# Kernel tuning notes

Measured on AMD Instinct MI355X. Metric: run time of the kernel, lower is better.

Reference implementation:

```python
import jax, jax.numpy as jnp
import numpy as np

N = 60000          # users
M = 40000          # items
NODES = N + M
D = 64             # embedding_dim
NLAYERS = 3        # layers = [64, 64, 64]
NNZ = 3_200_000    # nnz of L_I (avg degree 32)
B = 1024           # batch_size
NEG_SLOPE = 0.2


def setup_inputs() -> dict:
    key = jax.random.key(0)
    ks = jax.random.split(key, 12)
    edge_row = jax.random.randint(ks[0], (NNZ,), 0, NODES, dtype=jnp.int32)
    edge_col = jax.random.randint(ks[1], (NNZ,), 0, NODES, dtype=jnp.int32)
    # Laplacian values are small positive normalized weights
    edge_val = jax.random.uniform(ks[2], (NNZ,), dtype=jnp.float32) * (1.0 / 32.0)
    embed_user = jax.random.normal(ks[3], (N, D), dtype=jnp.float32) * 0.1
    embed_item = jax.random.normal(ks[4], (M, D), dtype=jnp.float32) * 0.1
    W1 = jax.random.normal(ks[5], (NLAYERS, D, D), dtype=jnp.float32) * 0.1
    W2 = jax.random.normal(ks[6], (NLAYERS, D, D), dtype=jnp.float32) * 0.1
    b1 = jax.random.normal(ks[7], (NLAYERS, 1, D), dtype=jnp.float32) * 0.1
    b2 = jax.random.normal(ks[8], (NLAYERS, 1, D), dtype=jnp.float32) * 0.1
    sampled_users = jax.random.randint(ks[9], (B,), 0, N, dtype=jnp.int32)
    observed_items_idx = jax.random.randint(ks[10], (B,), 0, M, dtype=jnp.int32)
    unobserved_items_idx = jax.random.randint(ks[11], (B,), 0, M, dtype=jnp.int32)
    return {
        "edge_row": edge_row, "edge_col": edge_col, "edge_val": edge_val,
        "embed_user": embed_user, "embed_item": embed_item,
        "W1": W1, "W2": W2, "b1": b1, "b2": b2,
        "sampled_users": sampled_users,
        "observed_items_idx": observed_items_idx,
        "unobserved_items_idx": unobserved_items_idx,
    }


def _spmm(row, col, val, x):
    # sparse (NODES x NODES) @ dense (NODES x D) via gather + segment-sum
    return jax.ops.segment_sum(val[:, None] * x[col], row, num_segments=NODES)


def reference(edge_row, edge_col, edge_val, embed_user, embed_item,
              W1, W2, b1, b2,
              sampled_users, observed_items_idx, unobserved_items_idx):
    x = jnp.concatenate([embed_user, embed_item], axis=0)  # (NODES, D)
    reprs = [x]
    for i in range(NLAYERS):
        lie = _spmm(edge_row, edge_col, edge_val, x)        # L_I @ E
        left = lie @ W1[i] + b1[i]
        right = (x * lie) @ W2[i] + b2[i]
        x = jax.nn.leaky_relu(left + right, negative_slope=NEG_SLOPE)
        reprs.append(x)
    final_reprs = jnp.concatenate(reprs, axis=1)            # (NODES, D*(NLAYERS+1))
    users_, items_ = final_reprs[:N], final_reprs[N:]
    return (users_[sampled_users],
            items_[observed_items_idx],
            items_[unobserved_items_idx])
```

## Files before the change

### kernel.cpp

```cpp
#include <hip/hip_runtime.h>

#define NN    60000
#define NODES 100000
#define DD    64
#define NNZ   3200000
#define BB    1024
#define NEG   0.2f
#define RPB   196
#define NBUCK 511
#define EPB   8192
#define NPB   ((NNZ + EPB - 1) / EPB)
#define CAP   7000
#define BCAP  7168
#define NSEG  13
#define KEYN  (NSEG * RPB)
#define SPB   (KEYN + 1)

__global__ __launch_bounds__(256) void k_init_x(const float* __restrict__ eu,
                                                const float* __restrict__ ei,
                                                float* __restrict__ x,
                                                int* __restrict__ gcur) {
    int i = blockIdx.x * 256 + threadIdx.x;
    if (i < NBUCK) gcur[i] = i * CAP;
    const int TOT = NODES * DD / 4;
    if (i >= TOT) return;
    const int UE = NN * DD / 4;
    float4 v = (i < UE) ? ((const float4*)eu)[i] : ((const float4*)ei)[i - UE];
    ((float4*)x)[i] = v;
}

__global__ __launch_bounds__(512) void k_place(const int* __restrict__ row,
                                               const int* __restrict__ col,
                                               const float* __restrict__ val,
                                               int* __restrict__ gcur,
                                               int2* __restrict__ bulk) {
    __shared__ int rows_l[EPB];
    __shared__ unsigned short perm[EPB];
    __shared__ int h[NBUCK], bloc[NBUCK], bcur[NBUCK], gseg[NBUCK];
    __shared__ int sc[512];
    int t = threadIdx.x;
    if (t < NBUCK) h[t] = 0;
    __syncthreads();
    int base = blockIdx.x * EPB;
    int n = min(EPB, NNZ - base);
    for (int k = t; k < n; k += 512) {
        int r = row[base + k];
        rows_l[k] = r;
        atomicAdd(&h[r / RPB], 1);
    }
    __syncthreads();
    {
        int v = (t < NBUCK) ? h[t] : 0;
        sc[t] = v;
        __syncthreads();
        for (int off = 1; off < 512; off <<= 1) {
            int u = (t >= off) ? sc[t - off] : 0;
            __syncthreads();
            sc[t] += u;
            __syncthreads();
        }
        if (t < NBUCK) {
            int ex = sc[t] - v;
            bloc[t] = ex;
            bcur[t] = ex;
            gseg[t] = v ? atomicAdd(&gcur[t], v) : 0;
        }
    }
    __syncthreads();
    for (int k = t; k < n; k += 512) {
        int p = atomicAdd(&bcur[rows_l[k] / RPB], 1);
        perm[p] = (unsigned short)k;
    }
    __syncthreads();
    for (int j = t; j < n; j += 512) {
        int k = perm[j];
        int r = rows_l[k];
        int b = r / RPB;
        int addr = gseg[b] + (j - bloc[b]);
        bulk[addr] = make_int2(((r - b * RPB) << 17) | col[base + k],
                               __float_as_int(val[base + k]));
    }
}

__global__ __launch_bounds__(512) void k_csr(const int* __restrict__ gcur,
                                             int2* __restrict__ bulk,
                                             int* __restrict__ starts) {
    __shared__ int2 eds[BCAP];
    __shared__ int cnt[KEYN], pos[KEYN];
    __shared__ int part[512];
    int b = blockIdx.x, t = threadIdx.x;
    int lo = b * CAP;
    int n = gcur[b] - lo;
    for (int k = t; k < KEYN; k += 512) cnt[k] = 0;
    __syncthreads();
    for (int i = t; i < n; i += 512) {
        int2 ed = bulk[lo + i];
        eds[i] = ed;
        int lr = ed.x >> 17, c = ed.x & 0x1FFFF;
        atomicAdd(&cnt[(c >> 13) * RPB + lr], 1);
    }
    __syncthreads();
    int run = 0;
#pragma unroll
    for (int j = 0; j < 5; ++j) {
        int k = t * 5 + j;
        if (k < KEYN) { pos[k] = run; run += cnt[k]; }
    }
    part[t] = run;
    __syncthreads();
    for (int off = 1; off < 512; off <<= 1) {
        int u = (t >= off) ? part[t - off] : 0;
        __syncthreads();
        part[t] += u;
        __syncthreads();
    }
    int poff = part[t] - run;
#pragma unroll
    for (int j = 0; j < 5; ++j) {
        int k = t * 5 + j;
        if (k < KEYN) pos[k] += poff;
    }
    __syncthreads();
    for (int k = t; k < KEYN; k += 512) {
        starts[b * SPB + k] = lo + pos[k];
        cnt[k] = pos[k];
    }
    if (t == 0) starts[b * SPB + KEYN] = lo + n;
    __syncthreads();
    for (int i = t; i < n; i += 512) {
        int2 ed = eds[i];
        int lr = ed.x >> 17, c = ed.x & 0x1FFFF;
        int p = atomicAdd(&cnt[(c >> 13) * RPB + lr], 1);
        bulk[lo + p] = ed;
    }
}

template <int PIPE>
__global__ __launch_bounds__(1024) void k_cspmm(const int* __restrict__ starts,
                                                const int2* __restrict__ cv,
                                                const float* __restrict__ x,
                                                float* __restrict__ lie) {
    __shared__ float acc[RPB * DD];
    int t = threadIdx.x, b = blockIdx.x;
    float4* av = (float4*)acc;
    for (int i = t; i < RPB * 16; i += 1024) av[i] = make_float4(0.f, 0.f, 0.f, 0.f);
    __syncthreads();
    int lane = t & 63;
    int wid = __builtin_amdgcn_readfirstlane(t >> 6);
    int r0 = (wid * RPB) >> 4;
    int r1 = ((wid + 1) * RPB) >> 4;
    int sb = b * SPB;
    for (int seg = 0; seg < NSEG; ++seg) {
        int s = starts[sb + seg * RPB + r0];
        int e = starts[sb + seg * RPB + r1];
        int cur = -1;
        float f = 0.f;
        if constexpr (PIPE == 0) {
            int g = s;
            for (; g + 8 <= e; g += 8) {
                int2 ee[8];
#pragma unroll
                for (int j = 0; j < 8; ++j) ee[j] = cv[g + j];
                float xv[8];
#pragma unroll
                for (int j = 0; j < 8; ++j) xv[j] = x[(ee[j].x & 0x1FFFF) * DD + lane];
#pragma unroll
                for (int j = 0; j < 8; ++j) {
                    int r = ee[j].x >> 17;
                    if (r != cur) {
                        if (cur >= 0) acc[cur * DD + lane] += f;
                        cur = r; f = 0.f;
                    }
                    f = fmaf(__int_as_float(ee[j].y), xv[j], f);
                }
            }
            for (; g < e; ++g) {
                int2 ed = cv[g];
                float xg = x[(ed.x & 0x1FFFF) * DD + lane];
                int r = ed.x >> 17;
                if (r != cur) {
                    if (cur >= 0) acc[cur * DD + lane] += f;
                    cur = r; f = 0.f;
                }
                f = fmaf(__int_as_float(ed.y), xg, f);
            }
        } else {
            int2 emA[8], emB[8];
            float xwA[8], xwB[8];
#define LDM(S, gg) { _Pragma("unroll") \
    for (int j = 0; j < 8; ++j) em##S[j] = cv[(gg) + j]; }
#define GTH(S) { _Pragma("unroll") \
    for (int j = 0; j < 8; ++j) xw##S[j] = x[(em##S[j].x & 0x1FFFF) * DD + lane]; }
#define CNS(S) { _Pragma("unroll") \
    for (int j = 0; j < 8; ++j) { \
        int r = em##S[j].x >> 17; \
        if (r != cur) { if (cur >= 0) acc[cur * DD + lane] += f; cur = r; f = 0.f; } \
        f = fmaf(__int_as_float(em##S[j].y), xw##S[j], f); } }
            int nb = (e - s) >> 3;
            if (nb > 0) {
                LDM(A, s) GTH(A)
                int ld = 1;
                for (;;) {
                    if (ld < nb) { LDM(B, s + ld * 8) GTH(B) ++ld; CNS(A) }
                    else         { CNS(A) break; }
                    if (ld < nb) { LDM(A, s + ld * 8) GTH(A) ++ld; CNS(B) }
                    else         { CNS(B) break; }
                }
            }
#undef LDM
#undef GTH
#undef CNS
            for (int g = s + nb * 8; g < e; ++g) {
                int2 ed = cv[g];
                float xg = x[(ed.x & 0x1FFFF) * DD + lane];
                int r = ed.x >> 17;
                if (r != cur) {
                    if (cur >= 0) acc[cur * DD + lane] += f;
                    cur = r; f = 0.f;
                }
                f = fmaf(__int_as_float(ed.y), xg, f);
            }
        }
        if (cur >= 0) acc[cur * DD + lane] += f;
    }
    __syncthreads();
    int row0 = b * RPB;
    for (int i = t; i < RPB * 16; i += 1024) {
        int gr = row0 + (i >> 4);
        if (gr < NODES) ((float4*)lie)[gr * 16 + (i & 15)] = av[i];
    }
}

__global__ __launch_bounds__(256) void k_gemm(float* __restrict__ x,
                                              const float* __restrict__ lie,
                                              const float* __restrict__ W1,
                                              const float* __restrict__ W2,
                                              const float* __restrict__ b1,
                                              const float* __restrict__ b2) {
    __shared__ float A1[64 * 64];
    __shared__ float A2[64 * 64];
    __shared__ float Ws1[64 * 64];
    __shared__ float Ws2[64 * 64];

    const int t = threadIdx.x;
    const int row0 = blockIdx.x * 64;

    {
        const float4* w1v = (const float4*)W1;
        const float4* w2v = (const float4*)W2;
        float4* s1v = (float4*)Ws1;
        float4* s2v = (float4*)Ws2;
#pragma unroll
        for (int q = 0; q < 4; ++q) {
            s1v[q * 256 + t] = w1v[q * 256 + t];
            s2v[q * 256 + t] = w2v[q * 256 + t];
        }
    }
#pragma unroll
    for (int q = 0; q < 4; ++q) {
        int f4 = q * 256 + t;
        int rl = f4 >> 4;
        int c4 = f4 & 15;
        int gr = row0 + rl;
        float4 lv = make_float4(0.f, 0.f, 0.f, 0.f);
        float4 xv = make_float4(0.f, 0.f, 0.f, 0.f);
        if (gr < NODES) {
            lv = *(const float4*)&lie[gr * DD + c4 * 4];
            xv = *(const float4*)&x[gr * DD + c4 * 4];
        }
        int sg = c4 ^ (rl & 15);
        ((float4*)A1)[rl * 16 + sg] = lv;
        ((float4*)A2)[rl * 16 + sg] = make_float4(lv.x * xv.x, lv.y * xv.y,
                                                  lv.z * xv.z, lv.w * xv.w);
    }
    __syncthreads();

    const int tx = t & 15;
    const int ty = t >> 4;
    float bs[4];
    {
        float4 bb1 = *(const float4*)&b1[tx * 4];
        float4 bb2 = *(const float4*)&b2[tx * 4];
        bs[0] = bb1.x + bb2.x; bs[1] = bb1.y + bb2.y;
        bs[2] = bb1.z + bb2.z; bs[3] = bb1.w + bb2.w;
    }
    float acc[4][4];
#pragma unroll
    for (int i = 0; i < 4; ++i)
#pragma unroll
        for (int j = 0; j < 4; ++j) acc[i][j] = bs[j];

    for (int k4 = 0; k4 < 16; ++k4) {
        float4 a1[4], a2[4];
#pragma unroll
        for (int i = 0; i < 4; ++i) {
            int r = ty * 4 + i;
            int sg = k4 ^ (r & 15);
            a1[i] = ((const float4*)A1)[r * 16 + sg];
            a2[i] = ((const float4*)A2)[r * 16 + sg];
        }
#pragma unroll
        for (int kk = 0; kk < 4; ++kk) {
            float4 w1 = ((const float4*)Ws1)[(k4 * 4 + kk) * 16 + tx];
            float4 w2 = ((const float4*)Ws2)[(k4 * 4 + kk) * 16 + tx];
#pragma unroll
            for (int i = 0; i < 4; ++i) {
                float av1 = (&a1[i].x)[kk];
                float av2 = (&a2[i].x)[kk];
                acc[i][0] = fmaf(av1, w1.x, fmaf(av2, w2.x, acc[i][0]));
                acc[i][1] = fmaf(av1, w1.y, fmaf(av2, w2.y, acc[i][1]));
                acc[i][2] = fmaf(av1, w1.z, fmaf(av2, w2.z, acc[i][2]));
                acc[i][3] = fmaf(av1, w1.w, fmaf(av2, w2.w, acc[i][3]));
            }
        }
    }
#pragma unroll
    for (int i = 0; i < 4; ++i) {
        int gr = row0 + ty * 4 + i;
        if (gr < NODES) {
            float4 o;
            o.x = acc[i][0] >= 0.f ? acc[i][0] : NEG * acc[i][0];
            o.y = acc[i][1] >= 0.f ? acc[i][1] : NEG * acc[i][1];
            o.z = acc[i][2] >= 0.f ? acc[i][2] : NEG * acc[i][2];
            o.w = acc[i][3] >= 0.f ? acc[i][3] : NEG * acc[i][3];
            *(float4*)&x[gr * DD + tx * 4] = o;
        }
    }
}

__global__ __launch_bounds__(256) void k_gather(const float* __restrict__ x,
                                                const int* __restrict__ su,
                                                const int* __restrict__ oi,
                                                const int* __restrict__ ui,
                                                float* __restrict__ out, int layer) {
    int w    = (blockIdx.x * 256 + threadIdx.x) >> 6;
    int lane = threadIdx.x & 63;
    if (w >= 3 * BB) return;
    int g = w >> 10, b = w & 1023;
    int node = (g == 0) ? su[b] : (NN + ((g == 1) ? oi[b] : ui[b]));
    out[w * 256 + layer * 64 + lane] = x[node * DD + lane];
}

extern "C" void kernel_launch(void* const* d_in, const int* in_sizes, int n_in,
                              void* d_out, int out_size, void* d_ws, size_t ws_size,
                              hipStream_t stream) {
    const int*   edge_row = (const int*)d_in[0];
    const int*   edge_col = (const int*)d_in[1];
    const float* edge_val = (const float*)d_in[2];
    const float* eu = (const float*)d_in[3];
    const float* ei = (const float*)d_in[4];
    const float* W1 = (const float*)d_in[5];
    const float* W2 = (const float*)d_in[6];
    const float* b1 = (const float*)d_in[7];
    const float* b2 = (const float*)d_in[8];
    const int*   su = (const int*)d_in[9];
    const int*   oi = (const int*)d_in[10];
    const int*   ui = (const int*)d_in[11];
    float* out = (float*)d_out;

    float* x      = (float*)d_ws;
    float* lie    = x + NODES * DD;
    int2*  bulk   = (int2*)(lie + NODES * DD);
    int*   gcur   = (int*)(bulk + NBUCK * CAP);
    int*   starts = gcur + NBUCK + 1;

    k_init_x<<<(NODES * DD / 4 + 255) / 256, 256, 0, stream>>>(eu, ei, x, gcur);
    k_gather<<<(3 * BB * 64 + 255) / 256, 256, 0, stream>>>(x, su, oi, ui, out, 0);

    k_place<<<NPB, 512, 0, stream>>>(edge_row, edge_col, edge_val, gcur, bulk);
    k_csr<<<NBUCK, 512, 0, stream>>>(gcur, bulk, starts);

    for (int l = 0; l < 3; ++l) {
        if (l == 1)
            k_cspmm<1><<<NBUCK, 1024, 0, stream>>>(starts, bulk, x, lie);
        else
            k_cspmm<0><<<NBUCK, 1024, 0, stream>>>(starts, bulk, x, lie);
        k_gemm<<<(NODES + 63) / 64, 256, 0, stream>>>(x, lie,
                                                      W1 + l * 4096, W2 + l * 4096,
                                                      b1 + l * 64,  b2 + l * 64);
        k_gather<<<(3 * BB * 64 + 255) / 256, 256, 0, stream>>>(x, su, oi, ui, out, l + 1);
    }
}
```

Before: 520.8 us.

## Fuse SpMM with dense layer transform using ping-pong x buffers

Merges the sparse aggregation kernel and the dense W1/W2 GEMM into one kernel. Each block computes its rows of L·E in shared memory and then applies both weight matrices, bias and leaky ReLU directly. Double-buffered x arrays replace the in-place update. This removes the lie intermediate round-trip through global memory and one launch per layer, and uses the pipelined gather variant for all layers. In exchange the GEMM stage now reads weights from global/L1 per FMA without register tiling and has fewer blocks (511) than the old GEMM kernel.

Measured after the change: 1.617 ms. 210% more time.

```diff
diff --git a/kernel.cpp b/kernel.cpp
--- a/kernel.cpp
+++ b/kernel.cpp
@@ -135,11 +135,14 @@
     }
 }
 
-template <int PIPE>
-__global__ __launch_bounds__(1024) void k_cspmm(const int* __restrict__ starts,
+__global__ __launch_bounds__(1024) void k_fused(const int* __restrict__ starts,
                                                 const int2* __restrict__ cv,
-                                                const float* __restrict__ x,
-                                                float* __restrict__ lie) {
+                                                const float* __restrict__ xs,
+                                                float* __restrict__ xd,
+                                                const float* __restrict__ W1,
+                                                const float* __restrict__ W2,
+                                                const float* __restrict__ b1,
+                                                const float* __restrict__ b2) {
     __shared__ float acc[RPB * DD];
     int t = threadIdx.x, b = blockIdx.x;
     float4* av = (float4*)acc;
@@ -155,175 +158,86 @@
         int e = starts[sb + seg * RPB + r1];
         int cur = -1;
         float f = 0.f;
-        if constexpr (PIPE == 0) {
-            int g = s;
-            for (; g + 8 <= e; g += 8) {
-                int2 ee[8];
-#pragma unroll
-                for (int j = 0; j < 8; ++j) ee[j] = cv[g + j];
-                float xv[8];
-#pragma unroll
-                for (int j = 0; j < 8; ++j) xv[j] = x[(ee[j].x & 0x1FFFF) * DD + lane];
-#pragma unroll
-                for (int j = 0; j < 8; ++j) {
-                    int r = ee[j].x >> 17;
-                    if (r != cur) {
-                        if (cur >= 0) acc[cur * DD + lane] += f;
-                        cur = r; f = 0.f;
-                    }
-                    f = fmaf(__int_as_float(ee[j].y), xv[j], f);
-                }
-            }
-            for (; g < e; ++g) {
-                int2 ed = cv[g];
-                float xg = x[(ed.x & 0x1FFFF) * DD + lane];
-                int r = ed.x >> 17;
-                if (r != cur) {
-                    if (cur >= 0) acc[cur * DD + lane] += f;
-                    cur = r; f = 0.f;
-                }
-                f = fmaf(__int_as_float(ed.y), xg, f);
-            }
-        } else {
-            int2 emA[8], emB[8];
-            float xwA[8], xwB[8];
+        int2 emA[8], emB[8];
+        float xwA[8], xwB[8];
 #define LDM(S, gg) { _Pragma("unroll") \
     for (int j = 0; j < 8; ++j) em##S[j] = cv[(gg) + j]; }
 #define GTH(S) { _Pragma("unroll") \
-    for (int j = 0; j < 8; ++j) xw##S[j] = x[(em##S[j].x & 0x1FFFF) * DD + lane]; }
+    for (int j = 0; j < 8; ++j) xw##S[j] = xs[(em##S[j].x & 0x1FFFF) * DD + lane]; }
 #define CNS(S) { _Pragma("unroll") \
     for (int j = 0; j < 8; ++j) { \
         int r = em##S[j].x >> 17; \
         if (r != cur) { if (cur >= 0) acc[cur * DD + lane] += f; cur = r; f = 0.f; } \
         f = fmaf(__int_as_float(em##S[j].y), xw##S[j], f); } }
-            int nb = (e - s) >> 3;
-            if (nb > 0) {
-                LDM(A, s) GTH(A)
-                int ld = 1;
-                for (;;) {
-                    if (ld < nb) { LDM(B, s + ld * 8) GTH(B) ++ld; CNS(A) }
-                    else         { CNS(A) break; }
-                    if (ld < nb) { LDM(A, s + ld * 8) GTH(A) ++ld; CNS(B) }
-                    else         { CNS(B) break; }
-                }
-            }
+        int nb = (e - s) >> 3;
+        if (nb > 0) {
+            LDM(A, s) GTH(A)
+            int ld = 1;
+            for (;;) {
+                if (ld < nb) { LDM(B, s + ld * 8) GTH(B) ++ld; CNS(A) }
+                else         { CNS(A) break; }
+                if (ld < nb) { LDM(A, s + ld * 8) GTH(A) ++ld; CNS(B) }
+                else         { CNS(B) break; }
+            }
+        }
 #undef LDM
 #undef GTH
 #undef CNS
-            for (int g = s + nb * 8; g < e; ++g) {
-                int2 ed = cv[g];
-                float xg = x[(ed.x & 0x1FFFF) * DD + lane];
-                int r = ed.x >> 17;
-                if (r != cur) {
-                    if (cur >= 0) acc[cur * DD + lane] += f;
-                    cur = r; f = 0.f;
-                }
-                f = fmaf(__int_as_float(ed.y), xg, f);
-            }
+        for (int g = s + nb * 8; g < e; ++g) {
+            int2 ed = cv[g];
+            float xg = xs[(ed.x & 0x1FFFF) * DD + lane];
+            int r = ed.x >> 17;
+            if (r != cur) {
+                if (cur >= 0) acc[cur * DD + lane] += f;
+                cur = r; f = 0.f;
+            }
+            f = fmaf(__int_as_float(ed.y), xg, f);
         }
         if (cur >= 0) acc[cur * DD + lane] += f;
     }
     __syncthreads();
-    int row0 = b * RPB;
-    for (int i = t; i < RPB * 16; i += 1024) {
-        int gr = row0 + (i >> 4);
-        if (gr < NODES) ((float4*)lie)[gr * 16 + (i & 15)] = av[i];
-    }
-}
-
-__global__ __launch_bounds__(256) void k_gemm(float* __restrict__ x,
-                                              const float* __restrict__ lie,
-                                              const float* __restrict__ W1,
-                                              const float* __restrict__ W2,
-                                              const float* __restrict__ b1,
-                                              const float* __restrict__ b2) {
-    __shared__ float A1[64 * 64];
-    __shared__ float A2[64 * 64];
-    __shared__ float Ws1[64 * 64];
-    __shared__ float Ws2[64 * 64];
-
-    const int t = threadIdx.x;
-    const int row0 = blockIdx.x * 64;
 
     {
+        const int row0 = b * RPB;
+        const int tx = t & 15;
+        const int ty = t >> 4;
         const float4* w1v = (const float4*)W1;
         const float4* w2v = (const float4*)W2;
-        float4* s1v = (float4*)Ws1;
-        float4* s2v = (float4*)Ws2;
-#pragma unroll
-        for (int q = 0; q < 4; ++q) {
-            s1v[q * 256 + t] = w1v[q * 256 + t];
-            s2v[q * 256 + t] = w2v[q * 256 + t];
-        }
-    }
-#pragma unroll
-    for (int q = 0; q < 4; ++q) {
-        int f4 = q * 256 + t;
-        int rl = f4 >> 4;
-        int c4 = f4 & 15;
-        int gr = row0 + rl;
-        float4 lv = make_float4(0.f, 0.f, 0.f, 0.f);
-        float4 xv = make_float4(0.f, 0.f, 0.f, 0.f);
-        if (gr < NODES) {
-            lv = *(const float4*)&lie[gr * DD + c4 * 4];
-            xv = *(const float4*)&x[gr * DD + c4 * 4];
-        }
-        int sg = c4 ^ (rl & 15);
-        ((float4*)A1)[rl * 16 + sg] = lv;
-        ((float4*)A2)[rl * 16 + sg] = make_float4(lv.x * xv.x, lv.y * xv.y,
-                                                  lv.z * xv.z, lv.w * xv.w);
-    }
-    __syncthreads();
-
-    const int tx = t & 15;
-    const int ty = t >> 4;
-    float bs[4];
-    {
-        float4 bb1 = *(const float4*)&b1[tx * 4];
-        float4 bb2 = *(const float4*)&b2[tx * 4];
-        bs[0] = bb1.x + bb2.x; bs[1] = bb1.y + bb2.y;
-        bs[2] = bb1.z + bb2.z; bs[3] = bb1.w + bb2.w;
-    }
-    float acc[4][4];
-#pragma unroll
-    for (int i = 0; i < 4; ++i)
-#pragma unroll
-        for (int j = 0; j < 4; ++j) acc[i][j] = bs[j];
-
-    for (int k4 = 0; k4 < 16; ++k4) {
-        float4 a1[4], a2[4];
-#pragma unroll
-        for (int i = 0; i < 4; ++i) {
-            int r = ty * 4 + i;
-            int sg = k4 ^ (r & 15);
-            a1[i] = ((const float4*)A1)[r * 16 + sg];
-            a2[i] = ((const float4*)A2)[r * 16 + sg];
-        }
-#pragma unroll
-        for (int kk = 0; kk < 4; ++kk) {
-            float4 w1 = ((const float4*)Ws1)[(k4 * 4 + kk) * 16 + tx];
-            float4 w2 = ((const float4*)Ws2)[(k4 * 4 + kk) * 16 + tx];
-#pragma unroll
-            for (int i = 0; i < 4; ++i) {
-                float av1 = (&a1[i].x)[kk];
-                float av2 = (&a2[i].x)[kk];
-                acc[i][0] = fmaf(av1, w1.x, fmaf(av2, w2.x, acc[i][0]));
-                acc[i][1] = fmaf(av1, w1.y, fmaf(av2, w2.y, acc[i][1]));
-                acc[i][2] = fmaf(av1, w1.z, fmaf(av2, w2.z, acc[i][2]));
-                acc[i][3] = fmaf(av1, w1.w, fmaf(av2, w2.w, acc[i][3]));
-            }
-        }
-    }
-#pragma unroll
-    for (int i = 0; i < 4; ++i) {
-        int gr = row0 + ty * 4 + i;
-        if (gr < NODES) {
-            float4 o;
-            o.x = acc[i][0] >= 0.f ? acc[i][0] : NEG * acc[i][0];
-            o.y = acc[i][1] >= 0.f ? acc[i][1] : NEG * acc[i][1];
-            o.z = acc[i][2] >= 0.f ? acc[i][2] : NEG * acc[i][2];
-            o.w = acc[i][3] >= 0.f ? acc[i][3] : NEG * acc[i][3];
-            *(float4*)&x[gr * DD + tx * 4] = o;
+        float4 b1v = ((const float4*)b1)[tx];
+        float4 b2v = ((const float4*)b2)[tx];
+        float4 bb = make_float4(b1v.x + b2v.x, b1v.y + b2v.y,
+                                b1v.z + b2v.z, b1v.w + b2v.w);
+        int nr = (ty < RPB - 192) ? 4 : 3;
+        for (int i = 0; i < nr; ++i) {
+            int lr = ty + i * 64;
+            int gr = row0 + lr;
+            bool live = (gr < NODES);
+            float4 o = bb;
+            const float4* lrow = (const float4*)&acc[lr * DD];
+            const float4* xrow = (const float4*)&xs[(live ? gr : 0) * DD];
+#pragma unroll
+            for (int k4 = 0; k4 < 16; ++k4) {
+                float4 l4 = lrow[k4];
+                float4 x4 = xrow[k4];
+#pragma unroll
+                for (int kk = 0; kk < 4; ++kk) {
+                    float lk = (&l4.x)[kk];
+                    float ak = lk * (&x4.x)[kk];
+                    float4 w1r = w1v[(k4 * 4 + kk) * 16 + tx];
+                    float4 w2r = w2v[(k4 * 4 + kk) * 16 + tx];
+                    o.x = fmaf(lk, w1r.x, fmaf(ak, w2r.x, o.x));
+                    o.y = fmaf(lk, w1r.y, fmaf(ak, w2r.y, o.y));
+                    o.z = fmaf(lk, w1r.z, fmaf(ak, w2r.z, o.z));
+                    o.w = fmaf(lk, w1r.w, fmaf(ak, w2r.w, o.w));
+                }
+            }
+            if (live) {
+                o.x = o.x >= 0.f ? o.x : NEG * o.x;
+                o.y = o.y >= 0.f ? o.y : NEG * o.y;
+                o.z = o.z >= 0.f ? o.z : NEG * o.z;
+                o.w = o.w >= 0.f ? o.w : NEG * o.w;
+                ((float4*)xd)[gr * 16 + tx] = o;
+            }
         }
     }
 }
@@ -358,26 +272,26 @@
     const int*   ui = (const int*)d_in[11];
     float* out = (float*)d_out;
 
-    float* x      = (float*)d_ws;
-    float* lie    = x + NODES * DD;
-    int2*  bulk   = (int2*)(lie + NODES * DD);
+    float* xa     = (float*)d_ws;
+    float* xb     = xa + NODES * DD;
+    int2*  bulk   = (int2*)(xb + NODES * DD);
     int*   gcur   = (int*)(bulk + NBUCK * CAP);
     int*   starts = gcur + NBUCK + 1;
 
-    k_init_x<<<(NODES * DD / 4 + 255) / 256, 256, 0, stream>>>(eu, ei, x, gcur);
-    k_gather<<<(3 * BB * 64 + 255) / 256, 256, 0, stream>>>(x, su, oi, ui, out, 0);
+    k_init_x<<<(NODES * DD / 4 + 255) / 256, 256, 0, stream>>>(eu, ei, xa, gcur);
+    k_gather<<<(3 * BB * 64 + 255) / 256, 256, 0, stream>>>(xa, su, oi, ui, out, 0);
 
     k_place<<<NPB, 512, 0, stream>>>(edge_row, edge_col, edge_val, gcur, bulk);
     k_csr<<<NBUCK, 512, 0, stream>>>(gcur, bulk, starts);
 
+    const float* xsrc = xa;
+    float*       xdst = xb;
     for (int l = 0; l < 3; ++l) {
-        if (l == 1)
-            k_cspmm<1><<<NBUCK, 1024, 0, stream>>>(starts, bulk, x, lie);
-        else
-            k_cspmm<0><<<NBUCK, 1024, 0, stream>>>(starts, bulk, x, lie);
-        k_gemm<<<(NODES + 63) / 64, 256, 0, stream>>>(x, lie,
-                                                      W1 + l * 4096, W2 + l * 4096,
-                                                      b1 + l * 64,  b2 + l * 64);
-        k_gather<<<(3 * BB * 64 + 255) / 256, 256, 0, stream>>>(x, su, oi, ui, out, l + 1);
-    }
-}
+        k_fused<<<NBUCK, 1024, 0, stream>>>(starts, bulk, xsrc, xdst,
+                                            W1 + l * 4096, W2 + l * 4096,
+                                            b1 + l * 64,  b2 + l * 64);
+        k_gather<<<(3 * BB * 64 + 255) / 256, 256, 0, stream>>>(xdst, su, oi, ui,
+                                                                out, l + 1);
+        const float* tmp = xsrc; xsrc = xdst; xdst = (float*)tmp;
+    }
+}
```
